# Performance work log

Hardware: AMD Instinct MI355X
Metric: run time of the kernel (lower is better)

## Reference

```python
import jax, jax.numpy as jnp
import numpy as np

B, S, H, I, E, K = 4, 2048, 1024, 4096, 8, 2


def setup_inputs() -> dict:
    key = jax.random.key(0)
    ks = jax.random.split(key, 6)
    x = jax.random.normal(ks[0], (B, S, H), dtype=jnp.float32)
    gate_w = jax.random.normal(ks[1], (H, E), dtype=jnp.float32) * 0.02
    up_w = jax.random.normal(ks[2], (E, H, I), dtype=jnp.float32) * 0.02
    up_b = jnp.zeros((E, I), dtype=jnp.float32)
    down_w = jax.random.normal(ks[3], (E, I, H), dtype=jnp.float32) * 0.02
    down_b = jnp.zeros((E, H), dtype=jnp.float32)
    return {"x": x, "gate_w": gate_w, "up_w": up_w, "up_b": up_b,
            "down_w": down_w, "down_b": down_b}


def reference(x, gate_w, up_w, up_b, down_w, down_b):
    # Router: logits [B,S,E], softmax probs
    logits = jnp.einsum('bsh,he->bse', x, gate_w)
    probs = jax.nn.softmax(logits, axis=-1)
    # top-k selection and renormalization of the selected probabilities
    topk_p, topk_idx = jax.lax.top_k(probs, K)            # [B,S,K]
    topk_p = topk_p / jnp.sum(topk_p, axis=-1, keepdims=True)
    # combine weights per expert: [B,S,E] (sum of renormalized top-k probs routed to e)
    combine = jnp.sum(jax.nn.one_hot(topk_idx, E, dtype=x.dtype) * topk_p[..., None], axis=2)
    # per-expert FFN, weighted combine (loop over fixed small expert set)
    out = jnp.zeros_like(x)
    for e in range(E):
        h = jax.nn.gelu(jnp.einsum('bsh,hi->bsi', x, up_w[e]) + up_b[e], approximate=False)
        y = jnp.einsum('bsi,ih->bsh', h, down_w[e]) + down_b[e]
        out = out + combine[..., e:e + 1] * y
    # aux statistics
    expert_usage = jnp.mean(probs, axis=(0, 1))           # [E]
    load_balance_loss = E * jnp.sum(expert_usage * expert_usage)
    top_expert = topk_idx[..., 0]                          # [B,S]
    return out, load_balance_loss, expert_usage, top_expert
```

## Files before the change

kernel.cpp:

```cpp
#include <hip/hip_runtime.h>
#include <cmath>

#define T_TOK 8192
#define HDIM 1024
#define IDIM 4096
#define NEXP 8

#define OFF_LOSS  8388608
#define OFF_USAGE 8388609
#define OFF_TOPE  8388617

typedef __attribute__((ext_vector_type(8))) short bf16x8;
typedef __attribute__((ext_vector_type(4))) float f32x4;
typedef unsigned short u16;
typedef unsigned int u32;

__device__ inline u16 f2bf(float f) {
  u32 u = __float_as_uint(f);
  u32 r = (u + 0x7FFFu + ((u >> 16) & 1u)) >> 16;
  return (u16)r;
}

__device__ inline void glds16(const void* g, void* l) {
  __builtin_amdgcn_global_load_lds(
      (const __attribute__((address_space(1))) u32*)g,
      (__attribute__((address_space(3))) u32*)l, 16, 0, 0);
}

__global__ __launch_bounds__(256)
void cvt_x(const float* __restrict__ x, u16* __restrict__ xb) {
  size_t i = ((size_t)blockIdx.x * 256 + threadIdx.x) * 8;
  float4 a = *(const float4*)(x + i);
  float4 b = *(const float4*)(x + i + 4);
  union { u16 s[8]; uint4 v; } u;
  u.s[0] = f2bf(a.x); u.s[1] = f2bf(a.y); u.s[2] = f2bf(a.z); u.s[3] = f2bf(a.w);
  u.s[4] = f2bf(b.x); u.s[5] = f2bf(b.y); u.s[6] = f2bf(b.z); u.s[7] = f2bf(b.w);
  *(uint4*)(xb + i) = u.v;
}

__global__ __launch_bounds__(256)
void transpose_cvt(const float* __restrict__ src, u16* __restrict__ dst, int R, int C) {
  __shared__ float tile[32][33];
  size_t eoff = (size_t)blockIdx.z * R * C;
  int r0 = blockIdx.y * 32, c0 = blockIdx.x * 32;
  int tx = threadIdx.x & 31, ty = threadIdx.x >> 5;
  const float* s = src + eoff;
  u16* d = dst + eoff;
#pragma unroll
  for (int k = 0; k < 4; k++)
    tile[ty + 8*k][tx] = s[(size_t)(r0 + ty + 8*k) * C + c0 + tx];
  __syncthreads();
#pragma unroll
  for (int k = 0; k < 4; k++)
    d[(size_t)(c0 + ty + 8*k) * R + r0 + tx] = f2bf(tile[tx][ty + 8*k]);
}

__global__ __launch_bounds__(64)
void router_kernel(const float* __restrict__ x, const float* __restrict__ gw,
                   float* __restrict__ probs, int* __restrict__ counts,
                   int* __restrict__ tlist, float* __restrict__ wlist,
                   float* __restrict__ out) {
  int tok = blockIdx.x;
  int lane = threadIdx.x;
  double acc[NEXP];
#pragma unroll
  for (int e = 0; e < NEXP; e++) acc[e] = 0.0;
  const float* xr = x + (size_t)tok * HDIM;
  for (int h = lane; h < HDIM; h += 64) {
    double xv = (double)xr[h];
    const float* g = gw + h * NEXP;
#pragma unroll
    for (int e = 0; e < NEXP; e++) acc[e] += xv * (double)g[e];
  }
#pragma unroll
  for (int off = 32; off > 0; off >>= 1) {
#pragma unroll
    for (int e = 0; e < NEXP; e++) acc[e] += __shfl_xor(acc[e], off);
  }
  if (lane == 0) {
    double m = acc[0];
#pragma unroll
    for (int e = 1; e < NEXP; e++) if (acc[e] > m) m = acc[e];
    double p[NEXP], ssum = 0.0;
#pragma unroll
    for (int e = 0; e < NEXP; e++) { p[e] = exp(acc[e] - m); ssum += p[e]; }
#pragma unroll
    for (int e = 0; e < NEXP; e++) p[e] /= ssum;
    int i1 = 0;
#pragma unroll
    for (int e = 1; e < NEXP; e++) if (p[e] > p[i1]) i1 = e;
    int i2 = (i1 == 0) ? 1 : 0;
#pragma unroll
    for (int e = 0; e < NEXP; e++) if (e != i1 && p[e] > p[i2]) i2 = e;
    double ps = p[i1] + p[i2];
#pragma unroll
    for (int e = 0; e < NEXP; e++) probs[(size_t)tok * NEXP + e] = (float)p[e];
    out[OFF_TOPE + tok] = (float)i1;
    int pos1 = atomicAdd(&counts[i1], 1);
    tlist[i1 * T_TOK + pos1] = tok;
    wlist[i1 * T_TOK + pos1] = (float)(p[i1] / ps);
    int pos2 = atomicAdd(&counts[i2], 1);
    tlist[i2 * T_TOK + pos2] = tok;
    wlist[i2 * T_TOK + pos2] = (float)(p[i2] / ps);
  }
}

__global__ void hbase_kernel(const int* __restrict__ counts, int* __restrict__ hbase) {
  if (threadIdx.x == 0 && blockIdx.x == 0) {
    int s = 0;
    for (int e = 0; e < NEXP; e++) { hbase[e] = s; s += counts[e]; }
    hbase[NEXP] = s;
  }
}

__global__ __launch_bounds__(256)
void usage_kernel(const float* __restrict__ probs, float* __restrict__ out) {
  int e = blockIdx.x;
  float s = 0.f;
  for (int t = threadIdx.x; t < T_TOK; t += 256) s += probs[(size_t)t * NEXP + e];
#pragma unroll
  for (int off = 32; off > 0; off >>= 1) s += __shfl_xor(s, off);
  __shared__ float red[4];
  int lane = threadIdx.x & 63, wid = threadIdx.x >> 6;
  if (lane == 0) red[wid] = s;
  __syncthreads();
  if (threadIdx.x == 0)
    out[OFF_USAGE + e] = (red[0] + red[1] + red[2] + red[3]) / (float)T_TOK;
}

__global__ void loss_kernel(float* __restrict__ out) {
  if (threadIdx.x == 0 && blockIdx.x == 0) {
    float s = 0.f;
    for (int e = 0; e < NEXP; e++) { float u = out[OFF_USAGE + e]; s += u * u; }
    out[OFF_LOSS] = (float)NEXP * s;
  }
}

__global__ __launch_bounds__(256, 2)
void up_gemm(const u16* __restrict__ xb, const u16* __restrict__ wbt,
             const float* __restrict__ bias, const int* __restrict__ counts,
             const int* __restrict__ hbase, const int* __restrict__ tlist,
             u16* __restrict__ hout, int e_fixed) {
  const int NT = IDIM / 128;
  const int MT = T_TOK / 128;
  int e, tm, tn;
  if (e_fixed >= 0) { e = e_fixed; tm = blockIdx.x / NT; tn = blockIdx.x % NT; }
  else { e = blockIdx.x / (MT * NT); int r = blockIdx.x % (MT * NT); tm = r / NT; tn = r % NT; }
  int cnt = counts[e];
  int m0 = tm * 128;
  if (m0 >= cnt) return;
  int hb = (e_fixed >= 0) ? 0 : hbase[e];
  int n0 = tn * 128;

  __shared__ u16 As[128 * 32];
  __shared__ u16 Bs[128 * 32];

  int t = threadIdx.x;
  int ra = t >> 2;
  int sw = (t & 3) ^ ((t >> 3) & 3);

  const int* tl = tlist + e * T_TOK;
  int g0 = m0 + ra;      if (g0 > cnt - 1) g0 = cnt - 1;
  int g1 = m0 + ra + 64; if (g1 > cnt - 1) g1 = cnt - 1;
  const u16* a0 = xb + (size_t)tl[g0] * HDIM + sw * 8;
  const u16* a1 = xb + (size_t)tl[g1] * HDIM + sw * 8;
  const u16* wb = wbt + (size_t)e * IDIM * HDIM;
  const u16* b0 = wb + (size_t)(n0 + ra) * HDIM + sw * 8;
  const u16* b1 = wb + (size_t)(n0 + ra + 64) * HDIM + sw * 8;

  u16* lA0 = &As[t * 8];
  u16* lA1 = &As[2048 + t * 8];
  u16* lB0 = &Bs[t * 8];
  u16* lB1 = &Bs[2048 + t * 8];

  f32x4 acc[4][4];
#pragma unroll
  for (int i = 0; i < 4; i++)
#pragma unroll
    for (int j = 0; j < 4; j++) acc[i][j] = (f32x4){0.f, 0.f, 0.f, 0.f};

  int lane = t & 63, wid = t >> 6;
  int wr = (wid >> 1) * 64, wc = (wid & 1) * 64;
  int lrow = lane & 15, lslot = lane >> 4;

  for (int k0 = 0; k0 < HDIM; k0 += 32) {
    __syncthreads();
    glds16(a0 + k0, lA0);
    glds16(a1 + k0, lA1);
    glds16(b0 + k0, lB0);
    glds16(b1 + k0, lB1);
    asm volatile("s_waitcnt vmcnt(0)" ::: "memory");
    __syncthreads();
    bf16x8 af[4], bfr[4];
#pragma unroll
    for (int mi = 0; mi < 4; mi++) {
      int row = wr + mi * 16 + lrow;
      af[mi] = *(const bf16x8*)&As[row * 32 + ((lslot ^ ((row >> 1) & 3)) * 8)];
    }
#pragma unroll
    for (int ni = 0; ni < 4; ni++) {
      int row = wc + ni * 16 + lrow;
      bfr[ni] = *(const bf16x8*)&Bs[row * 32 + ((lslot ^ ((row >> 1) & 3)) * 8)];
    }
#pragma unroll
    for (int mi = 0; mi < 4; mi++)
#pragma unroll
      for (int ni = 0; ni < 4; ni++)
        acc[mi][ni] = __builtin_amdgcn_mfma_f32_16x16x32_bf16(af[mi], bfr[ni], acc[mi][ni], 0, 0, 0);
  }

  float bv[4];
#pragma unroll
  for (int ni = 0; ni < 4; ni++)
    bv[ni] = bias[(size_t)e * IDIM + n0 + wc + ni * 16 + lrow];
  int r4 = lslot * 4;
#pragma unroll
  for (int mi = 0; mi < 4; mi++) {
    int rb = m0 + wr + mi * 16 + r4;
#pragma unroll
    for (int j = 0; j < 4; j++) {
      int row = rb + j;
      if (row < cnt) {
        u16* hp = hout + (size_t)(hb + row) * IDIM + n0 + wc + lrow;
#pragma unroll
        for (int ni = 0; ni < 4; ni++) {
          float v = acc[mi][ni][j] + bv[ni];
          float gl = 0.5f * v * (1.0f + erff(v * 0.70710678118654752f));
          hp[ni * 16] = f2bf(gl);
        }
      }
    }
  }
}

__global__ __launch_bounds__(256, 2)
void down_gemm(const u16* __restrict__ h, const u16* __restrict__ wbt,
               const float* __restrict__ bias, const int* __restrict__ counts,
               const int* __restrict__ hbase, const int* __restrict__ tlist,
               const float* __restrict__ wlist, float* __restrict__ out, int e_fixed) {
  const int NT = HDIM / 128;
  const int MT = T_TOK / 128;
  int e, tm, tn;
  if (e_fixed >= 0) { e = e_fixed; tm = blockIdx.x / NT; tn = blockIdx.x % NT; }
  else { e = blockIdx.x / (MT * NT); int r = blockIdx.x % (MT * NT); tm = r / NT; tn = r % NT; }
  int cnt = counts[e];
  int m0 = tm * 128;
  if (m0 >= cnt) return;
  int hb = (e_fixed >= 0) ? 0 : hbase[e];
  int n0 = tn * 128;

  __shared__ u16 As[128 * 32];
  __shared__ u16 Bs[128 * 32];

  int t = threadIdx.x;
  int ra = t >> 2;
  int sw = (t & 3) ^ ((t >> 3) & 3);

  int g0 = m0 + ra;      if (g0 > cnt - 1) g0 = cnt - 1;
  int g1 = m0 + ra + 64; if (g1 > cnt - 1) g1 = cnt - 1;
  const u16* a0 = h + (size_t)(hb + g0) * IDIM + sw * 8;
  const u16* a1 = h + (size_t)(hb + g1) * IDIM + sw * 8;
  const u16* wb = wbt + (size_t)e * HDIM * IDIM;
  const u16* b0 = wb + (size_t)(n0 + ra) * IDIM + sw * 8;
  const u16* b1 = wb + (size_t)(n0 + ra + 64) * IDIM + sw * 8;

  u16* lA0 = &As[t * 8];
  u16* lA1 = &As[2048 + t * 8];
  u16* lB0 = &Bs[t * 8];
  u16* lB1 = &Bs[2048 + t * 8];

  f32x4 acc[4][4];
#pragma unroll
  for (int i = 0; i < 4; i++)
#pragma unroll
    for (int j = 0; j < 4; j++) acc[i][j] = (f32x4){0.f, 0.f, 0.f, 0.f};

  int lane = t & 63, wid = t >> 6;
  int wr = (wid >> 1) * 64, wc = (wid & 1) * 64;
  int lrow = lane & 15, lslot = lane >> 4;

  for (int k0 = 0; k0 < IDIM; k0 += 32) {
    __syncthreads();
    glds16(a0 + k0, lA0);
    glds16(a1 + k0, lA1);
    glds16(b0 + k0, lB0);
    glds16(b1 + k0, lB1);
    asm volatile("s_waitcnt vmcnt(0)" ::: "memory");
    __syncthreads();
    bf16x8 af[4], bfr[4];
#pragma unroll
    for (int mi = 0; mi < 4; mi++) {
      int row = wr + mi * 16 + lrow;
      af[mi] = *(const bf16x8*)&As[row * 32 + ((lslot ^ ((row >> 1) & 3)) * 8)];
    }
#pragma unroll
    for (int ni = 0; ni < 4; ni++) {
      int row = wc + ni * 16 + lrow;
      bfr[ni] = *(const bf16x8*)&Bs[row * 32 + ((lslot ^ ((row >> 1) & 3)) * 8)];
    }
#pragma unroll
    for (int mi = 0; mi < 4; mi++)
#pragma unroll
      for (int ni = 0; ni < 4; ni++)
        acc[mi][ni] = __builtin_amdgcn_mfma_f32_16x16x32_bf16(af[mi], bfr[ni], acc[mi][ni], 0, 0, 0);
  }

  float bv[4];
#pragma unroll
  for (int ni = 0; ni < 4; ni++)
    bv[ni] = bias[(size_t)e * HDIM + n0 + wc + ni * 16 + lrow];
  int r4 = lslot * 4;
#pragma unroll
  for (int mi = 0; mi < 4; mi++) {
    int rb = m0 + wr + mi * 16 + r4;
#pragma unroll
    for (int j = 0; j < 4; j++) {
      int row = rb + j;
      if (row < cnt) {
        int tok = tlist[e * T_TOK + row];
        float w = wlist[e * T_TOK + row];
        float* op = out + (size_t)tok * HDIM + n0 + wc + lrow;
#pragma unroll
        for (int ni = 0; ni < 4; ni++)
          atomicAdd(&op[ni * 16], w * (acc[mi][ni][j] + bv[ni]));
      }
    }
  }
}

extern "C" void kernel_launch(void* const* d_in, const int* in_sizes, int n_in,
                              void* d_out, int out_size, void* d_ws, size_t ws_size,
                              hipStream_t stream) {
  const float* x   = (const float*)d_in[0];
  const float* gw  = (const float*)d_in[1];
  const float* upw = (const float*)d_in[2];
  const float* upb = (const float*)d_in[3];
  const float* dnw = (const float*)d_in[4];
  const float* dnb = (const float*)d_in[5];
  float* out = (float*)d_out;
  char* ws = (char*)d_ws;

  int*   counts = (int*)(ws + 0);
  int*   hbase  = (int*)(ws + 64);
  int*   tlist  = (int*)(ws + 256);
  float* wlist  = (float*)(ws + 256 + 262144);
  float* probs  = (float*)(ws + 256 + 2 * 262144);
  u16*   xb     = (u16*)(ws + 1048576);
  u16*   upbt   = (u16*)(ws + 1048576 + 16777216);
  u16*   dnbt   = (u16*)(ws + 1048576 + 16777216 + 67108864ull);
  u16*   hbuf   = (u16*)(ws + 1048576 + 16777216 + 2ull * 67108864ull);

  bool grouped = ws_size >= 286261248ull;

  hipMemsetAsync(counts, 0, 32, stream);
  hipMemsetAsync(d_out, 0, (size_t)out_size * 4, stream);

  cvt_x<<<4096, 256, 0, stream>>>(x, xb);
  transpose_cvt<<<dim3(IDIM / 32, HDIM / 32, NEXP), 256, 0, stream>>>(upw, upbt, HDIM, IDIM);
  transpose_cvt<<<dim3(HDIM / 32, IDIM / 32, NEXP), 256, 0, stream>>>(dnw, dnbt, IDIM, HDIM);
  router_kernel<<<T_TOK, 64, 0, stream>>>(x, gw, probs, counts, tlist, wlist, out);
  hbase_kernel<<<1, 64, 0, stream>>>(counts, hbase);
  usage_kernel<<<NEXP, 256, 0, stream>>>(probs, out);
  loss_kernel<<<1, 64, 0, stream>>>(out);

  if (grouped) {
    up_gemm<<<NEXP * 64 * 32, 256, 0, stream>>>(xb, upbt, upb, counts, hbase, tlist, hbuf, -1);
    down_gemm<<<NEXP * 64 * 8, 256, 0, stream>>>(hbuf, dnbt, dnb, counts, hbase, tlist, wlist, out, -1);
  } else {
    for (int e = 0; e < NEXP; e++) {
      up_gemm<<<64 * 32, 256, 0, stream>>>(xb, upbt, upb, counts, hbase, tlist, hbuf, e);
      down_gemm<<<64 * 8, 256, 0, stream>>>(hbuf, dnbt, dnb, counts, hbase, tlist, wlist, out, e);
    }
  }
}
```

Before: 803.6 us.

## Use 256x256 tiles, double-buffered LDS and XCD-aware block remap in expert GEMMs

Both expert GEMMs move from 128x128 tiles with 256 threads to 256x256 tiles with 512 threads (8 waves, each computing 128x64). LDS is double-buffered so the next K-slice's global-to-LDS loads are issued before the MFMAs on the current slice, removing the per-iteration load-then-wait stall. Block indices are remapped so consecutive tiles land on the same XCD for better L2 reuse. In exchange, register pressure roughly doubles (32 accumulators per wave), and larger tiles waste more work on partially filled expert row tiles.

```diff
diff --git a/kernel.cpp b/kernel.cpp
--- a/kernel.cpp
+++ b/kernel.cpp
@@ -136,77 +136,88 @@
   }
 }
 
-__global__ __launch_bounds__(256, 2)
+
+__global__ __launch_bounds__(512, 2)
 void up_gemm(const u16* __restrict__ xb, const u16* __restrict__ wbt,
              const float* __restrict__ bias, const int* __restrict__ counts,
              const int* __restrict__ hbase, const int* __restrict__ tlist,
              u16* __restrict__ hout, int e_fixed) {
-  const int NT = IDIM / 128;
-  const int MT = T_TOK / 128;
+  const int NT = IDIM / 256;
+  const int MT = T_TOK / 256;
+  int nwg = gridDim.x;
+  int q = nwg >> 3;
+  int orig = blockIdx.x;
+  int wg = (orig & 7) * q + (orig >> 3);
   int e, tm, tn;
-  if (e_fixed >= 0) { e = e_fixed; tm = blockIdx.x / NT; tn = blockIdx.x % NT; }
-  else { e = blockIdx.x / (MT * NT); int r = blockIdx.x % (MT * NT); tm = r / NT; tn = r % NT; }
+  if (e_fixed >= 0) { e = e_fixed; tm = wg / NT; tn = wg % NT; }
+  else { e = wg / (MT * NT); int r = wg % (MT * NT); tm = r / NT; tn = r % NT; }
   int cnt = counts[e];
-  int m0 = tm * 128;
+  int m0 = tm * 256;
   if (m0 >= cnt) return;
   int hb = (e_fixed >= 0) ? 0 : hbase[e];
-  int n0 = tn * 128;
-
-  __shared__ u16 As[128 * 32];
-  __shared__ u16 Bs[128 * 32];
+  int n0 = tn * 256;
+
+  __shared__ u16 As[2 * 8192];
+  __shared__ u16 Bs[2 * 8192];
 
   int t = threadIdx.x;
-  int ra = t >> 2;
-  int sw = (t & 3) ^ ((t >> 3) & 3);
+  int r0 = t >> 2, r1 = r0 + 128;
+  int c0 = (t & 3) ^ ((r0 >> 1) & 3);
+  int c1 = (t & 3) ^ ((r1 >> 1) & 3);
 
   const int* tl = tlist + e * T_TOK;
-  int g0 = m0 + ra;      if (g0 > cnt - 1) g0 = cnt - 1;
-  int g1 = m0 + ra + 64; if (g1 > cnt - 1) g1 = cnt - 1;
-  const u16* a0 = xb + (size_t)tl[g0] * HDIM + sw * 8;
-  const u16* a1 = xb + (size_t)tl[g1] * HDIM + sw * 8;
+  int ga0 = m0 + r0; if (ga0 > cnt - 1) ga0 = cnt - 1;
+  int ga1 = m0 + r1; if (ga1 > cnt - 1) ga1 = cnt - 1;
+  const u16* pa0 = xb + (size_t)tl[ga0] * HDIM + c0 * 8;
+  const u16* pa1 = xb + (size_t)tl[ga1] * HDIM + c1 * 8;
   const u16* wb = wbt + (size_t)e * IDIM * HDIM;
-  const u16* b0 = wb + (size_t)(n0 + ra) * HDIM + sw * 8;
-  const u16* b1 = wb + (size_t)(n0 + ra + 64) * HDIM + sw * 8;
-
-  u16* lA0 = &As[t * 8];
-  u16* lA1 = &As[2048 + t * 8];
-  u16* lB0 = &Bs[t * 8];
-  u16* lB1 = &Bs[2048 + t * 8];
-
-  f32x4 acc[4][4];
-#pragma unroll
-  for (int i = 0; i < 4; i++)
+  const u16* pb0 = wb + (size_t)(n0 + r0) * HDIM + c0 * 8;
+  const u16* pb1 = wb + (size_t)(n0 + r1) * HDIM + c1 * 8;
+
+  f32x4 acc[8][4];
+#pragma unroll
+  for (int i = 0; i < 8; i++)
 #pragma unroll
     for (int j = 0; j < 4; j++) acc[i][j] = (f32x4){0.f, 0.f, 0.f, 0.f};
 
   int lane = t & 63, wid = t >> 6;
-  int wr = (wid >> 1) * 64, wc = (wid & 1) * 64;
+  int wr = (wid >> 2) * 128, wc = (wid & 3) * 64;
   int lrow = lane & 15, lslot = lane >> 4;
 
-  for (int k0 = 0; k0 < HDIM; k0 += 32) {
-    __syncthreads();
-    glds16(a0 + k0, lA0);
-    glds16(a1 + k0, lA1);
-    glds16(b0 + k0, lB0);
-    glds16(b1 + k0, lB1);
+  auto stage = [&](int b, int k0) {
+    glds16(pa0 + k0, &As[b * 8192 + t * 8]);
+    glds16(pa1 + k0, &As[b * 8192 + (t + 512) * 8]);
+    glds16(pb0 + k0, &Bs[b * 8192 + t * 8]);
+    glds16(pb1 + k0, &Bs[b * 8192 + (t + 512) * 8]);
+  };
+
+  stage(0, 0);
+  asm volatile("s_waitcnt vmcnt(0)" ::: "memory");
+  __syncthreads();
+
+  const int nk = HDIM / 32;
+  int cur = 0;
+  for (int kt = 0; kt < nk; ++kt) {
+    if (kt + 1 < nk) stage(cur ^ 1, (kt + 1) * 32);
+    bf16x8 af[8], bfv[4];
+#pragma unroll
+    for (int mi = 0; mi < 8; mi++) {
+      int row = wr + mi * 16 + lrow;
+      af[mi] = *(const bf16x8*)&As[cur * 8192 + row * 32 + ((lslot ^ ((row >> 1) & 3)) * 8)];
+    }
+#pragma unroll
+    for (int ni = 0; ni < 4; ni++) {
+      int row = wc + ni * 16 + lrow;
+      bfv[ni] = *(const bf16x8*)&Bs[cur * 8192 + row * 32 + ((lslot ^ ((row >> 1) & 3)) * 8)];
+    }
+#pragma unroll
+    for (int mi = 0; mi < 8; mi++)
+#pragma unroll
+      for (int ni = 0; ni < 4; ni++)
+        acc[mi][ni] = __builtin_amdgcn_mfma_f32_16x16x32_bf16(af[mi], bfv[ni], acc[mi][ni], 0, 0, 0);
     asm volatile("s_waitcnt vmcnt(0)" ::: "memory");
     __syncthreads();
-    bf16x8 af[4], bfr[4];
-#pragma unroll
-    for (int mi = 0; mi < 4; mi++) {
-      int row = wr + mi * 16 + lrow;
-      af[mi] = *(const bf16x8*)&As[row * 32 + ((lslot ^ ((row >> 1) & 3)) * 8)];
-    }
-#pragma unroll
-    for (int ni = 0; ni < 4; ni++) {
-      int row = wc + ni * 16 + lrow;
-      bfr[ni] = *(const bf16x8*)&Bs[row * 32 + ((lslot ^ ((row >> 1) & 3)) * 8)];
-    }
-#pragma unroll
-    for (int mi = 0; mi < 4; mi++)
-#pragma unroll
-      for (int ni = 0; ni < 4; ni++)
-        acc[mi][ni] = __builtin_amdgcn_mfma_f32_16x16x32_bf16(af[mi], bfr[ni], acc[mi][ni], 0, 0, 0);
+    cur ^= 1;
   }
 
   float bv[4];
@@ -215,7 +226,7 @@
     bv[ni] = bias[(size_t)e * IDIM + n0 + wc + ni * 16 + lrow];
   int r4 = lslot * 4;
 #pragma unroll
-  for (int mi = 0; mi < 4; mi++) {
+  for (int mi = 0; mi < 8; mi++) {
     int rb = m0 + wr + mi * 16 + r4;
 #pragma unroll
     for (int j = 0; j < 4; j++) {
@@ -233,76 +244,86 @@
   }
 }
 
-__global__ __launch_bounds__(256, 2)
+__global__ __launch_bounds__(512, 2)
 void down_gemm(const u16* __restrict__ h, const u16* __restrict__ wbt,
                const float* __restrict__ bias, const int* __restrict__ counts,
                const int* __restrict__ hbase, const int* __restrict__ tlist,
                const float* __restrict__ wlist, float* __restrict__ out, int e_fixed) {
-  const int NT = HDIM / 128;
-  const int MT = T_TOK / 128;
+  const int NT = HDIM / 256;
+  const int MT = T_TOK / 256;
+  int nwg = gridDim.x;
+  int q = nwg >> 3;
+  int orig = blockIdx.x;
+  int wg = (orig & 7) * q + (orig >> 3);
   int e, tm, tn;
-  if (e_fixed >= 0) { e = e_fixed; tm = blockIdx.x / NT; tn = blockIdx.x % NT; }
-  else { e = blockIdx.x / (MT * NT); int r = blockIdx.x % (MT * NT); tm = r / NT; tn = r % NT; }
+  if (e_fixed >= 0) { e = e_fixed; tm = wg / NT; tn = wg % NT; }
+  else { e = wg / (MT * NT); int r = wg % (MT * NT); tm = r / NT; tn = r % NT; }
   int cnt = counts[e];
-  int m0 = tm * 128;
+  int m0 = tm * 256;
   if (m0 >= cnt) return;
   int hb = (e_fixed >= 0) ? 0 : hbase[e];
-  int n0 = tn * 128;
-
-  __shared__ u16 As[128 * 32];
-  __shared__ u16 Bs[128 * 32];
+  int n0 = tn * 256;
+
+  __shared__ u16 As[2 * 8192];
+  __shared__ u16 Bs[2 * 8192];
 
   int t = threadIdx.x;
-  int ra = t >> 2;
-  int sw = (t & 3) ^ ((t >> 3) & 3);
-
-  int g0 = m0 + ra;      if (g0 > cnt - 1) g0 = cnt - 1;
-  int g1 = m0 + ra + 64; if (g1 > cnt - 1) g1 = cnt - 1;
-  const u16* a0 = h + (size_t)(hb + g0) * IDIM + sw * 8;
-  const u16* a1 = h + (size_t)(hb + g1) * IDIM + sw * 8;
+  int r0 = t >> 2, r1 = r0 + 128;
+  int c0 = (t & 3) ^ ((r0 >> 1) & 3);
+  int c1 = (t & 3) ^ ((r1 >> 1) & 3);
+
+  int ga0 = m0 + r0; if (ga0 > cnt - 1) ga0 = cnt - 1;
+  int ga1 = m0 + r1; if (ga1 > cnt - 1) ga1 = cnt - 1;
+  const u16* pa0 = h + (size_t)(hb + ga0) * IDIM + c0 * 8;
+  const u16* pa1 = h + (size_t)(hb + ga1) * IDIM + c1 * 8;
   const u16* wb = wbt + (size_t)e * HDIM * IDIM;
-  const u16* b0 = wb + (size_t)(n0 + ra) * IDIM + sw * 8;
-  const u16* b1 = wb + (size_t)(n0 + ra + 64) * IDIM + sw * 8;
-
-  u16* lA0 = &As[t * 8];
-  u16* lA1 = &As[2048 + t * 8];
-  u16* lB0 = &Bs[t * 8];
-  u16* lB1 = &Bs[2048 + t * 8];
-
-  f32x4 acc[4][4];
-#pragma unroll
-  for (int i = 0; i < 4; i++)
+  const u16* pb0 = wb + (size_t)(n0 + r0) * IDIM + c0 * 8;
+  const u16* pb1 = wb + (size_t)(n0 + r1) * IDIM + c1 * 8;
+
+  f32x4 acc[8][4];
+#pragma unroll
+  for (int i = 0; i < 8; i++)
 #pragma unroll
     for (int j = 0; j < 4; j++) acc[i][j] = (f32x4){0.f, 0.f, 0.f, 0.f};
 
   int lane = t & 63, wid = t >> 6;
-  int wr = (wid >> 1) * 64, wc = (wid & 1) * 64;
+  int wr = (wid >> 2) * 128, wc = (wid & 3) * 64;
   int lrow = lane & 15, lslot = lane >> 4;
 
-  for (int k0 = 0; k0 < IDIM; k0 += 32) {
-    __syncthreads();
-    glds16(a0 + k0, lA0);
-    glds16(a1 + k0, lA1);
-    glds16(b0 + k0, lB0);
-    glds16(b1 + k0, lB1);
+  auto stage = [&](int b, int k0) {
+    glds16(pa0 + k0, &As[b * 8192 + t * 8]);
+    glds16(pa1 + k0, &As[b * 8192 + (t + 512) * 8]);
+    glds16(pb0 + k0, &Bs[b * 8192 + t * 8]);
+    glds16(pb1 + k0, &Bs[b * 8192 + (t + 512) * 8]);
+  };
+
+  stage(0, 0);
+  asm volatile("s_waitcnt vmcnt(0)" ::: "memory");
+  __syncthreads();
+
+  const int nk = IDIM / 32;
+  int cur = 0;
+  for (int kt = 0; kt < nk; ++kt) {
+    if (kt + 1 < nk) stage(cur ^ 1, (kt + 1) * 32);
+    bf16x8 af[8], bfv[4];
+#pragma unroll
+    for (int mi = 0; mi < 8; mi++) {
+      int row = wr + mi * 16 + lrow;
+      af[mi] = *(const bf16x8*)&As[cur * 8192 + row * 32 + ((lslot ^ ((row >> 1) & 3)) * 8)];
+    }
+#pragma unroll
+    for (int ni = 0; ni < 4; ni++) {
+      int row = wc + ni * 16 + lrow;
+      bfv[ni] = *(const bf16x8*)&Bs[cur * 8192 + row * 32 + ((lslot ^ ((row >> 1) & 3)) * 8)];
+    }
+#pragma unroll
+    for (int mi = 0; mi < 8; mi++)
+#pragma unroll
+      for (int ni = 0; ni < 4; ni++)
+        acc[mi][ni] = __builtin_amdgcn_mfma_f32_16x16x32_bf16(af[mi], bfv[ni], acc[mi][ni], 0, 0, 0);
     asm volatile("s_waitcnt vmcnt(0)" ::: "memory");
     __syncthreads();
-    bf16x8 af[4], bfr[4];
-#pragma unroll
-    for (int mi = 0; mi < 4; mi++) {
-      int row = wr + mi * 16 + lrow;
-      af[mi] = *(const bf16x8*)&As[row * 32 + ((lslot ^ ((row >> 1) & 3)) * 8)];
-    }
-#pragma unroll
-    for (int ni = 0; ni < 4; ni++) {
-      int row = wc + ni * 16 + lrow;
-      bfr[ni] = *(const bf16x8*)&Bs[row * 32 + ((lslot ^ ((row >> 1) & 3)) * 8)];
-    }
-#pragma unroll
-    for (int mi = 0; mi < 4; mi++)
-#pragma unroll
-      for (int ni = 0; ni < 4; ni++)
-        acc[mi][ni] = __builtin_amdgcn_mfma_f32_16x16x32_bf16(af[mi], bfr[ni], acc[mi][ni], 0, 0, 0);
+    cur ^= 1;
   }
 
   float bv[4];
@@ -311,7 +332,7 @@
     bv[ni] = bias[(size_t)e * HDIM + n0 + wc + ni * 16 + lrow];
   int r4 = lslot * 4;
 #pragma unroll
-  for (int mi = 0; mi < 4; mi++) {
+  for (int mi = 0; mi < 8; mi++) {
     int rb = m0 + wr + mi * 16 + r4;
 #pragma unroll
     for (int j = 0; j < 4; j++) {
@@ -364,12 +385,12 @@
   loss_kernel<<<1, 64, 0, stream>>>(out);
 
   if (grouped) {
-    up_gemm<<<NEXP * 64 * 32, 256, 0, stream>>>(xb, upbt, upb, counts, hbase, tlist, hbuf, -1);
-    down_gemm<<<NEXP * 64 * 8, 256, 0, stream>>>(hbuf, dnbt, dnb, counts, hbase, tlist, wlist, out, -1);
+    up_gemm<<<NEXP * 32 * 16, 512, 0, stream>>>(xb, upbt, upb, counts, hbase, tlist, hbuf, -1);
+    down_gemm<<<NEXP * 32 * 4, 512, 0, stream>>>(hbuf, dnbt, dnb, counts, hbase, tlist, wlist, out, -1);
   } else {
     for (int e = 0; e < NEXP; e++) {
-      up_gemm<<<64 * 32, 256, 0, stream>>>(xb, upbt, upb, counts, hbase, tlist, hbuf, e);
-      down_gemm<<<64 * 8, 256, 0, stream>>>(hbuf, dnbt, dnb, counts, hbase, tlist, wlist, out, e);
-    }
-  }
-}
+      up_gemm<<<32 * 16, 512, 0, stream>>>(xb, upbt, upb, counts, hbase, tlist, hbuf, e);
+      down_gemm<<<32 * 4, 512, 0, stream>>>(hbuf, dnbt, dnb, counts, hbase, tlist, wlist, out, e);
+    }
+  }
+}
```

Result: slower. 1.019 ms (+26.8%).

## Triple-buffer LDS with async prefetch and XCD-aware block remap in expert GEMMs

Applied to the files above, without the earlier changes.

Both up and down expert GEMMs now use a 3-stage LDS ring buffer. Global-to-LDS loads for tile k+2 are issued before computing tile k, and the loop waits with a partial vmcnt instead of draining all loads each step. Block indices are remapped so that consecutive logical tiles land on the same XCD, which should improve L2 reuse of weights, and launch bounds are raised to 3 blocks per CU. Tripling LDS use and asking for higher occupancy may spill registers or cap residency, and the single barrier per step depends on the ring depth to avoid overwrite races.

```diff
diff --git a/kernel.cpp b/kernel.cpp
--- a/kernel.cpp
+++ b/kernel.cpp
@@ -136,42 +136,41 @@
   }
 }
 
-__global__ __launch_bounds__(256, 2)
+
+__global__ __launch_bounds__(256, 3)
 void up_gemm(const u16* __restrict__ xb, const u16* __restrict__ wbt,
              const float* __restrict__ bias, const int* __restrict__ counts,
              const int* __restrict__ hbase, const int* __restrict__ tlist,
              u16* __restrict__ hout, int e_fixed) {
   const int NT = IDIM / 128;
   const int MT = T_TOK / 128;
+  int q = gridDim.x >> 3;
+  int orig = blockIdx.x;
+  int wg = (orig & 7) * q + (orig >> 3);
   int e, tm, tn;
-  if (e_fixed >= 0) { e = e_fixed; tm = blockIdx.x / NT; tn = blockIdx.x % NT; }
-  else { e = blockIdx.x / (MT * NT); int r = blockIdx.x % (MT * NT); tm = r / NT; tn = r % NT; }
+  if (e_fixed >= 0) { e = e_fixed; tm = wg / NT; tn = wg % NT; }
+  else { e = wg / (MT * NT); int r = wg % (MT * NT); tm = r / NT; tn = r % NT; }
   int cnt = counts[e];
   int m0 = tm * 128;
   if (m0 >= cnt) return;
   int hb = (e_fixed >= 0) ? 0 : hbase[e];
   int n0 = tn * 128;
 
-  __shared__ u16 As[128 * 32];
-  __shared__ u16 Bs[128 * 32];
+  __shared__ u16 As[3 * 4096];
+  __shared__ u16 Bs[3 * 4096];
 
   int t = threadIdx.x;
   int ra = t >> 2;
-  int sw = (t & 3) ^ ((t >> 3) & 3);
+  int sw = (t & 3) ^ ((ra >> 1) & 3);
 
   const int* tl = tlist + e * T_TOK;
   int g0 = m0 + ra;      if (g0 > cnt - 1) g0 = cnt - 1;
   int g1 = m0 + ra + 64; if (g1 > cnt - 1) g1 = cnt - 1;
-  const u16* a0 = xb + (size_t)tl[g0] * HDIM + sw * 8;
-  const u16* a1 = xb + (size_t)tl[g1] * HDIM + sw * 8;
+  const u16* pa0 = xb + (size_t)tl[g0] * HDIM + sw * 8;
+  const u16* pa1 = xb + (size_t)tl[g1] * HDIM + sw * 8;
   const u16* wb = wbt + (size_t)e * IDIM * HDIM;
-  const u16* b0 = wb + (size_t)(n0 + ra) * HDIM + sw * 8;
-  const u16* b1 = wb + (size_t)(n0 + ra + 64) * HDIM + sw * 8;
-
-  u16* lA0 = &As[t * 8];
-  u16* lA1 = &As[2048 + t * 8];
-  u16* lB0 = &Bs[t * 8];
-  u16* lB1 = &Bs[2048 + t * 8];
+  const u16* pb0 = wb + (size_t)(n0 + ra) * HDIM + sw * 8;
+  const u16* pb1 = wb + (size_t)(n0 + ra + 64) * HDIM + sw * 8;
 
   f32x4 acc[4][4];
 #pragma unroll
@@ -183,31 +182,52 @@
   int wr = (wid >> 1) * 64, wc = (wid & 1) * 64;
   int lrow = lane & 15, lslot = lane >> 4;
 
-  for (int k0 = 0; k0 < HDIM; k0 += 32) {
-    __syncthreads();
-    glds16(a0 + k0, lA0);
-    glds16(a1 + k0, lA1);
-    glds16(b0 + k0, lB0);
-    glds16(b1 + k0, lB1);
-    asm volatile("s_waitcnt vmcnt(0)" ::: "memory");
-    __syncthreads();
-    bf16x8 af[4], bfr[4];
+  auto stage = [&](int b, int k0) {
+    u16* a = &As[b * 4096];
+    u16* bb = &Bs[b * 4096];
+    glds16(pa0 + k0, a + t * 8);
+    glds16(pa1 + k0, a + 2048 + t * 8);
+    glds16(pb0 + k0, bb + t * 8);
+    glds16(pb1 + k0, bb + 2048 + t * 8);
+  };
+  auto compute = [&](int b) {
+    const u16* A = &As[b * 4096];
+    const u16* Bb = &Bs[b * 4096];
+    bf16x8 af[4], bfv[4];
 #pragma unroll
     for (int mi = 0; mi < 4; mi++) {
       int row = wr + mi * 16 + lrow;
-      af[mi] = *(const bf16x8*)&As[row * 32 + ((lslot ^ ((row >> 1) & 3)) * 8)];
+      af[mi] = *(const bf16x8*)&A[row * 32 + ((lslot ^ ((row >> 1) & 3)) * 8)];
     }
 #pragma unroll
     for (int ni = 0; ni < 4; ni++) {
       int row = wc + ni * 16 + lrow;
-      bfr[ni] = *(const bf16x8*)&Bs[row * 32 + ((lslot ^ ((row >> 1) & 3)) * 8)];
+      bfv[ni] = *(const bf16x8*)&Bb[row * 32 + ((lslot ^ ((row >> 1) & 3)) * 8)];
     }
 #pragma unroll
     for (int mi = 0; mi < 4; mi++)
 #pragma unroll
       for (int ni = 0; ni < 4; ni++)
-        acc[mi][ni] = __builtin_amdgcn_mfma_f32_16x16x32_bf16(af[mi], bfr[ni], acc[mi][ni], 0, 0, 0);
-  }
+        acc[mi][ni] = __builtin_amdgcn_mfma_f32_16x16x32_bf16(af[mi], bfv[ni], acc[mi][ni], 0, 0, 0);
+  };
+
+  const int nk = HDIM / 32;
+  stage(0, 0);
+  stage(1, 32);
+  int cur = 0;
+  for (int kt = 0; kt < nk - 1; ++kt) {
+    asm volatile("s_waitcnt vmcnt(4)" ::: "memory");
+    __builtin_amdgcn_s_barrier();
+    if (kt + 2 < nk) {
+      int nxt = cur + 2; if (nxt >= 3) nxt -= 3;
+      stage(nxt, (kt + 2) * 32);
+    }
+    compute(cur);
+    cur = (cur == 2) ? 0 : cur + 1;
+  }
+  asm volatile("s_waitcnt vmcnt(0)" ::: "memory");
+  __builtin_amdgcn_s_barrier();
+  compute(cur);
 
   float bv[4];
 #pragma unroll
@@ -233,41 +253,39 @@
   }
 }
 
-__global__ __launch_bounds__(256, 2)
+__global__ __launch_bounds__(256, 3)
 void down_gemm(const u16* __restrict__ h, const u16* __restrict__ wbt,
                const float* __restrict__ bias, const int* __restrict__ counts,
                const int* __restrict__ hbase, const int* __restrict__ tlist,
                const float* __restrict__ wlist, float* __restrict__ out, int e_fixed) {
   const int NT = HDIM / 128;
   const int MT = T_TOK / 128;
+  int q = gridDim.x >> 3;
+  int orig = blockIdx.x;
+  int wg = (orig & 7) * q + (orig >> 3);
   int e, tm, tn;
-  if (e_fixed >= 0) { e = e_fixed; tm = blockIdx.x / NT; tn = blockIdx.x % NT; }
-  else { e = blockIdx.x / (MT * NT); int r = blockIdx.x % (MT * NT); tm = r / NT; tn = r % NT; }
+  if (e_fixed >= 0) { e = e_fixed; tm = wg / NT; tn = wg % NT; }
+  else { e = wg / (MT * NT); int r = wg % (MT * NT); tm = r / NT; tn = r % NT; }
   int cnt = counts[e];
   int m0 = tm * 128;
   if (m0 >= cnt) return;
   int hb = (e_fixed >= 0) ? 0 : hbase[e];
   int n0 = tn * 128;
 
-  __shared__ u16 As[128 * 32];
-  __shared__ u16 Bs[128 * 32];
+  __shared__ u16 As[3 * 4096];
+  __shared__ u16 Bs[3 * 4096];
 
   int t = threadIdx.x;
   int ra = t >> 2;
-  int sw = (t & 3) ^ ((t >> 3) & 3);
+  int sw = (t & 3) ^ ((ra >> 1) & 3);
 
   int g0 = m0 + ra;      if (g0 > cnt - 1) g0 = cnt - 1;
   int g1 = m0 + ra + 64; if (g1 > cnt - 1) g1 = cnt - 1;
-  const u16* a0 = h + (size_t)(hb + g0) * IDIM + sw * 8;
-  const u16* a1 = h + (size_t)(hb + g1) * IDIM + sw * 8;
+  const u16* pa0 = h + (size_t)(hb + g0) * IDIM + sw * 8;
+  const u16* pa1 = h + (size_t)(hb + g1) * IDIM + sw * 8;
   const u16* wb = wbt + (size_t)e * HDIM * IDIM;
-  const u16* b0 = wb + (size_t)(n0 + ra) * IDIM + sw * 8;
-  const u16* b1 = wb + (size_t)(n0 + ra + 64) * IDIM + sw * 8;
-
-  u16* lA0 = &As[t * 8];
-  u16* lA1 = &As[2048 + t * 8];
-  u16* lB0 = &Bs[t * 8];
-  u16* lB1 = &Bs[2048 + t * 8];
+  const u16* pb0 = wb + (size_t)(n0 + ra) * IDIM + sw * 8;
+  const u16* pb1 = wb + (size_t)(n0 + ra + 64) * IDIM + sw * 8;
 
   f32x4 acc[4][4];
 #pragma unroll
@@ -279,31 +297,52 @@
   int wr = (wid >> 1) * 64, wc = (wid & 1) * 64;
   int lrow = lane & 15, lslot = lane >> 4;
 
-  for (int k0 = 0; k0 < IDIM; k0 += 32) {
-    __syncthreads();
-    glds16(a0 + k0, lA0);
-    glds16(a1 + k0, lA1);
-    glds16(b0 + k0, lB0);
-    glds16(b1 + k0, lB1);
-    asm volatile("s_waitcnt vmcnt(0)" ::: "memory");
-    __syncthreads();
-    bf16x8 af[4], bfr[4];
+  auto stage = [&](int b, int k0) {
+    u16* a = &As[b * 4096];
+    u16* bb = &Bs[b * 4096];
+    glds16(pa0 + k0, a + t * 8);
+    glds16(pa1 + k0, a + 2048 + t * 8);
+    glds16(pb0 + k0, bb + t * 8);
+    glds16(pb1 + k0, bb + 2048 + t * 8);
+  };
+  auto compute = [&](int b) {
+    const u16* A = &As[b * 4096];
+    const u16* Bb = &Bs[b * 4096];
+    bf16x8 af[4], bfv[4];
 #pragma unroll
     for (int mi = 0; mi < 4; mi++) {
       int row = wr + mi * 16 + lrow;
-      af[mi] = *(const bf16x8*)&As[row * 32 + ((lslot ^ ((row >> 1) & 3)) * 8)];
+      af[mi] = *(const bf16x8*)&A[row * 32 + ((lslot ^ ((row >> 1) & 3)) * 8)];
     }
 #pragma unroll
     for (int ni = 0; ni < 4; ni++) {
       int row = wc + ni * 16 + lrow;
-      bfr[ni] = *(const bf16x8*)&Bs[row * 32 + ((lslot ^ ((row >> 1) & 3)) * 8)];
+      bfv[ni] = *(const bf16x8*)&Bb[row * 32 + ((lslot ^ ((row >> 1) & 3)) * 8)];
     }
 #pragma unroll
     for (int mi = 0; mi < 4; mi++)
 #pragma unroll
       for (int ni = 0; ni < 4; ni++)
-        acc[mi][ni] = __builtin_amdgcn_mfma_f32_16x16x32_bf16(af[mi], bfr[ni], acc[mi][ni], 0, 0, 0);
-  }
+        acc[mi][ni] = __builtin_amdgcn_mfma_f32_16x16x32_bf16(af[mi], bfv[ni], acc[mi][ni], 0, 0, 0);
+  };
+
+  const int nk = IDIM / 32;
+  stage(0, 0);
+  stage(1, 32);
+  int cur = 0;
+  for (int kt = 0; kt < nk - 1; ++kt) {
+    asm volatile("s_waitcnt vmcnt(4)" ::: "memory");
+    __builtin_amdgcn_s_barrier();
+    if (kt + 2 < nk) {
+      int nxt = cur + 2; if (nxt >= 3) nxt -= 3;
+      stage(nxt, (kt + 2) * 32);
+    }
+    compute(cur);
+    cur = (cur == 2) ? 0 : cur + 1;
+  }
+  asm volatile("s_waitcnt vmcnt(0)" ::: "memory");
+  __builtin_amdgcn_s_barrier();
+  compute(cur);
 
   float bv[4];
 #pragma unroll
```

Measured after the change: 848.1 us. 1.06x slower.
